# Optimization experiments

Measured on AMD Instinct MI355X. Metric: run time of the kernel, lower is better.

The kernel has to match this reference:

```python
import jax, jax.numpy as jnp
import numpy as np

DECAY = 0.99
EPS = 1e-5
BETA = 0.25

def _l2norm(v, axis=-1):
    # F.normalize: x / max(||x||, 1e-12)
    n = jnp.sqrt(jnp.sum(v * v, axis=axis, keepdims=True))
    return v / jnp.maximum(n, 1e-12)

def setup_inputs() -> dict:
    key = jax.random.key(0)
    k0, k1, k2, k3 = jax.random.split(key, 4)
    B, C, H, W, E, K = 8, 256, 64, 64, 32, 8192
    x = jax.random.normal(k0, (B, C, H, W), jnp.float32)
    Wq = jax.random.normal(k1, (E, C), jnp.float32) * 0.05  # 1x1 conv kernel
    bq = jnp.zeros((E,), jnp.float32)
    emb = jax.random.normal(k2, (K, E), jnp.float32)
    emb = _l2norm(emb, axis=1)  # matches F.normalize init in __init__
    ema_cluster_size = jnp.ones((K,), jnp.float32)
    ema_weight = emb  # consistent post-init EMA state
    return {"x": x, "Wq": Wq, "bq": bq, "embedding": emb,
            "ema_cluster_size": ema_cluster_size, "ema_weight": ema_weight}

def reference(x, Wq, bq, embedding, ema_cluster_size, ema_weight):
    B, C, H, W = x.shape
    E = Wq.shape[0]
    K = embedding.shape[0]
    # quant_conv: 1x1 conv == per-pixel linear
    z = jnp.einsum('bchw,ec->behw', x, Wq) + bq[None, :, None, None]  # [B,E,H,W]
    z_flat = z.transpose(0, 2, 3, 1).reshape(-1, E)  # [N,E]
    # get_idx(use_znorm=True): cosine similarity argmax (== argmin L2 on normalized)
    zn = _l2norm(z_flat, axis=1)
    en = _l2norm(embedding, axis=1)
    indices = jnp.argmax(zn @ en.T, axis=1)  # [N]
    # codebook gather (raw embedding, as in torch)
    z_q = embedding[indices].reshape(B, H, W, E).transpose(0, 3, 1, 2)  # [B,E,H,W]
    # EMA update (training path; scatter == one-hot.T @ z_flat / one-hot.sum)
    counts = jax.ops.segment_sum(jnp.ones((z_flat.shape[0],), z_flat.dtype), indices, num_segments=K)
    dw = jax.ops.segment_sum(z_flat, indices, num_segments=K)  # [K,E]
    new_cs = DECAY * ema_cluster_size + (1.0 - DECAY) * counts
    new_w = DECAY * ema_weight + (1.0 - DECAY) * dw
    n = jnp.sum(new_cs)
    cs_smoothed = (new_cs + EPS) / (n + K * EPS) * n
    new_embedding = new_w / cs_smoothed[:, None]
    # commitment loss + straight-through
    qloss = BETA * jnp.mean((jax.lax.stop_gradient(z_q) - z) ** 2)
    z_q_st = z + jax.lax.stop_gradient(z_q - z)
    return (z_q_st, indices.reshape(B, H, W), qloss, new_embedding, new_cs, new_w)
```

## Files before the change

kernel.cpp:

```cpp
#include <hip/hip_runtime.h>

#define B_ 8
#define C_ 256
#define HW_ 4096
#define E_ 32
#define K_ 8192
#define N_ 32768
#define NCHUNK 4
#define KC_ (K_ / NCHUNK)
#define NSTAGE (KC_ / 128)
#define KSEG 32
#define PIX 128

#define DECAY_ 0.99f
#define OMD_   0.01f
#define EPS_   1e-5f
#define BETA_  0.25f

#define O_ZQ   0
#define O_IDX  1048576
#define O_QL   1081344
#define O_NEMB 1081345
#define O_NCS  1343489
#define O_NW   1351681

#define WS_EH   0u
#define WS_EM   131072u
#define WS_Z    262144u
#define WS_PACK 1310720u
#define WS_PCS  1572864u
#define WS_QP   1572992u

typedef float f32x4 __attribute__((ext_vector_type(4)));
typedef short s16x8 __attribute__((ext_vector_type(8)));
typedef unsigned long long u64;

__device__ __forceinline__ unsigned short f2bf(float f) {
    unsigned u = __float_as_uint(f);
    u = u + 0x7fffu + ((u >> 16) & 1u);
    return (unsigned short)(u >> 16);
}
__device__ __forceinline__ float bf2f(unsigned short h) {
    return __uint_as_float(((unsigned)h) << 16);
}
__device__ __forceinline__ unsigned ford(float f) {
    unsigned u = __float_as_uint(f);
    return (u & 0x80000000u) ? ~u : (u | 0x80000000u);
}
__device__ __forceinline__ int imax(int a, int b) { return a > b ? a : b; }
__device__ __forceinline__ int imin(int a, int b) { return a < b ? a : b; }

__device__ __forceinline__ void gload_lds16(const void* g, void* l) {
    __builtin_amdgcn_global_load_lds(
        (const __attribute__((address_space(1))) unsigned int*)g,
        (__attribute__((address_space(3))) unsigned int*)l, 16, 0, 0);
}

__global__ __launch_bounds__(512) void k_pre(const float* __restrict__ emb,
                                             const float* __restrict__ cs,
                                             uint4* __restrict__ eh16,
                                             uint4* __restrict__ em16,
                                             float* __restrict__ part_cs,
                                             const float* __restrict__ x,
                                             const float* __restrict__ Wq,
                                             const float* __restrict__ bq,
                                             float* __restrict__ zout) {
    __shared__ float wqt[C_ * E_];
    __shared__ float red8[8];
    int tid = threadIdx.x;

    if (blockIdx.x < 16) {
        int k = blockIdx.x * 512 + tid;
        const float4* r = (const float4*)(emb + (size_t)k * E_);
        float v[E_];
        float ss = 0.f;
#pragma unroll
        for (int i = 0; i < 8; i++) {
            float4 t = r[i];
            v[i*4+0] = t.x; v[i*4+1] = t.y; v[i*4+2] = t.z; v[i*4+3] = t.w;
            ss += t.x*t.x + t.y*t.y + t.z*t.z + t.w*t.w;
        }
        float inv = 1.0f / fmaxf(sqrtf(ss), 1e-12f);
        unsigned short h1a[E_], h2a[E_];
#pragma unroll
        for (int e = 0; e < E_; e++) {
            float en = v[e] * inv;
            unsigned short h1 = f2bf(en);
            float r1 = en - bf2f(h1);
            h1a[e] = h1; h2a[e] = f2bf(r1);
        }
        int t = k >> 4, c15 = k & 15;
#pragma unroll
        for (int i = 0; i < 4; i++) {
            eh16[t * 64 + i * 16 + c15] = ((uint4*)h1a)[i];
            em16[t * 64 + i * 16 + c15] = ((uint4*)h2a)[i];
        }

        float cv = cs[blockIdx.x * 512 + tid];
#pragma unroll
        for (int off = 32; off > 0; off >>= 1) cv += __shfl_down(cv, off);
        int lane = tid & 63, wid = tid >> 6;
        if (lane == 0) red8[wid] = cv;
        __syncthreads();
        if (tid == 0) {
            float s = 0.f;
#pragma unroll
            for (int i = 0; i < 8; i++) s += red8[i];
            part_cs[blockIdx.x] = s;
        }
        return;
    }

    int zb = blockIdx.x - 16;
#pragma unroll
    for (int i = 0; i < 16; i++) {
        int g = i * 512 + tid;
        int e = g >> 8;
        int c = g & 255;
        wqt[c * E_ + e] = Wq[g];
    }
    __syncthreads();
    int lp = tid & 63, eg = tid >> 6;
    int n0 = zb * 128 + lp;
    int b  = n0 >> 12, hw = n0 & (HW_ - 1);
    const float* xp = x + (size_t)b * C_ * HW_ + hw;
    float a[8];
#pragma unroll
    for (int j = 0; j < 8; j++) a[j] = 0.f;
#pragma unroll 4
    for (int c = 0; c < C_; c++) {
        float xa = xp[(size_t)c * HW_];
        float xb = xp[(size_t)c * HW_ + 64];
        float4 wv = *(const float4*)(wqt + c * E_ + eg * 4);
        a[0] += xa * wv.x; a[1] += xa * wv.y; a[2] += xa * wv.z; a[3] += xa * wv.w;
        a[4] += xb * wv.x; a[5] += xb * wv.y; a[6] += xb * wv.z; a[7] += xb * wv.w;
    }
    float bq0 = bq[eg*4+0], bq1v = bq[eg*4+1], bq2v = bq[eg*4+2], bq3 = bq[eg*4+3];
    *(float4*)(zout + (size_t)n0 * E_ + eg * 4) =
        make_float4(a[0]+bq0, a[1]+bq1v, a[2]+bq2v, a[3]+bq3);
    *(float4*)(zout + (size_t)(n0 + 64) * E_ + eg * 4) =
        make_float4(a[4]+bq0, a[5]+bq1v, a[6]+bq2v, a[7]+bq3);
}

__global__ __launch_bounds__(512) void k_score_mfma(const float* __restrict__ zws,
                                                    const char* __restrict__ ehb,
                                                    const char* __restrict__ emb_b,
                                                    int2* __restrict__ pk2) {
    __shared__ __align__(16) char smem[32768];

    int tid  = threadIdx.x;
    int lane = tid & 63;
    int w    = tid >> 6;
    int chunk = blockIdx.y;

    s16x8 a1, a2;
    {
        int ploc = w * 16 + (lane & 15);
        int n0   = blockIdx.x * PIX + ploc;
        int e0   = (lane >> 4) * 8;
        const float4* zp = (const float4*)(zws + (size_t)n0 * E_ + e0);
        float4 z0 = zp[0], z1 = zp[1];
        float zz[8] = {z0.x, z0.y, z0.z, z0.w, z1.x, z1.y, z1.z, z1.w};
#pragma unroll
        for (int j = 0; j < 8; j++) {
            float zv = zz[j] * 134217728.0f;
            unsigned short h1 = f2bf(zv);
            float r1 = zv - bf2f(h1);
            a1[j] = (short)h1; a2[j] = (short)f2bf(r1);
        }
    }

    const char* srcp[2];
#pragma unroll
    for (int i = 0; i < 2; i++) {
        int d = i * 512 + tid;
        int pl = d >> 9, dd = d & 511;
        srcp[i] = (pl ? emb_b : ehb) + (size_t)chunk * (KC_ * 64) + dd * 16;
    }

#pragma unroll
    for (int i = 0; i < 2; i++)
        gload_lds16(srcp[i], smem + (i * 512 + tid) * 16);
    __syncthreads();

    int rbase = 8191 - chunk * KC_ - (lane & 15);
    int bq1[4], bq2[4];
#pragma unroll
    for (int j = 0; j < 4; j++) { bq1[j] = (int)0x80000000; bq2[j] = (int)0x80000000; }
    f32x4 zero4 = {0.f, 0.f, 0.f, 0.f};

    for (int st = 0; st < NSTAGE; st++) {
        if (st + 1 < NSTAGE) {
            char* dst = smem + ((st + 1) & 1) * 16384;
#pragma unroll
            for (int i = 0; i < 2; i++)
                gload_lds16(srcp[i] + (size_t)(st + 1) * 8192, dst + (i * 512 + tid) * 16);
        }
        const char* cur = smem + (st & 1) * 16384;
        int rst = rbase - st * 128;

#pragma unroll
        for (int g = 0; g < 2; g++) {
            int ct = g * 4;
            s16x8 b1[4], b2[4];
#pragma unroll
            for (int q = 0; q < 4; q++) {
                b1[q] = ((const s16x8*)(cur +        (ct + q) * 1024))[lane];
                b2[q] = ((const s16x8*)(cur + 8192 + (ct + q) * 1024))[lane];
            }
            f32x4 acc[4];
#pragma unroll
            for (int q = 0; q < 4; q++)
                acc[q] = __builtin_amdgcn_mfma_f32_16x16x32_bf16(a1, b1[q], zero4, 0, 0, 0);
#pragma unroll
            for (int q = 0; q < 4; q++)
                acc[q] = __builtin_amdgcn_mfma_f32_16x16x32_bf16(a1, b2[q], acc[q], 0, 0, 0);
#pragma unroll
            for (int q = 0; q < 4; q++)
                acc[q] = __builtin_amdgcn_mfma_f32_16x16x32_bf16(a2, b1[q], acc[q], 0, 0, 0);
            int r0 = rst - ct * 16;
#pragma unroll
            for (int j = 0; j < 4; j++) {
                int v0 = ((int)acc[0][j] & (int)0xFFFFE000) | r0;
                int v1 = ((int)acc[1][j] & (int)0xFFFFE000) | (r0 - 16);
                int v2 = ((int)acc[2][j] & (int)0xFFFFE000) | (r0 - 32);
                int v3 = ((int)acc[3][j] & (int)0xFFFFE000) | (r0 - 48);
                int hi = imax(imax(v0, v1), imax(v2, v3));
                int m  = imin(bq1[j], hi);
                bq1[j] = imax(bq1[j], hi);
                bq2[j] = imax(bq2[j], m);
            }
        }
        __syncthreads();
    }

#pragma unroll
    for (int off = 1; off < 16; off <<= 1) {
#pragma unroll
        for (int j = 0; j < 4; j++) {
            int o1 = __shfl_xor(bq1[j], off, 64);
            int o2 = __shfl_xor(bq2[j], off, 64);
            int m  = imin(bq1[j], o1);
            bq1[j] = imax(bq1[j], o1);
            bq2[j] = imax(imax(bq2[j], o2), m);
        }
    }
    if ((lane & 15) == 0) {
        int rowbase = blockIdx.x * PIX + w * 16 + (lane >> 4) * 4;
#pragma unroll
        for (int j = 0; j < 4; j++)
            pk2[(size_t)chunk * N_ + rowbase + j] = make_int2(bq1[j], bq2[j]);
    }
}

__device__ __forceinline__ float rescore(const float* __restrict__ emb, int k,
                                         const float* zrow) {
    const float4* r = (const float4*)(emb + (size_t)k * E_);
    float4 v[8];
    float ss = 0.f;
#pragma unroll
    for (int i = 0; i < 8; i++) {
        v[i] = r[i];
        ss += v[i].x * v[i].x + v[i].y * v[i].y + v[i].z * v[i].z + v[i].w * v[i].w;
    }
    float inv = 1.0f / fmaxf(sqrtf(ss), 1e-12f);
    const float4* zp = (const float4*)zrow;
    float sx = 0.f, sy = 0.f, sz = 0.f, sw = 0.f;
#pragma unroll
    for (int i = 0; i < 8; i++) {
        float4 e4 = make_float4(v[i].x * inv, v[i].y * inv, v[i].z * inv, v[i].w * inv);
        float4 zr = zp[i];
        sx += zr.x * e4.x; sy += zr.y * e4.y;
        sz += zr.z * e4.z; sw += zr.w * e4.w;
    }
    return (sx + sy) + (sz + sw);
}

__global__ __launch_bounds__(256) void k_scatter(const float* __restrict__ zws,
                                                 const int2* __restrict__ pk2,
                                                 const float* __restrict__ emb,
                                                 float* __restrict__ out_zq,
                                                 float* __restrict__ out_idx,
                                                 float* __restrict__ qpart) {
    __shared__ float zbuf[32 * E_];
    __shared__ int   idxs_s[32];
    __shared__ float red[4];
    int tid = threadIdx.x;

    const float4* zsrc = (const float4*)(zws + (size_t)blockIdx.x * 32 * E_);
    ((float4*)zbuf)[tid] = zsrc[tid];
    __syncthreads();

    {
        int p = tid >> 3, c8 = tid & 7;
        int chunk = c8 >> 1, top = c8 & 1;
        int nn = blockIdx.x * 32 + p;
        int2 c2 = pk2[(size_t)chunk * N_ + nn];
        int raw = top ? c2.y : c2.x;
        int k = 8191 - (raw & 0x1fff);
        k = k < 0 ? 0 : (k > K_ - 1 ? K_ - 1 : k);
        float s = rescore(emb, k, zbuf + p * E_);
        u64 pkd = ((u64)ford(s) << 32) | (unsigned)(K_ - 1 - k);
        u64 o = __shfl_xor(pkd, 1, 64); pkd = pkd > o ? pkd : o;
        o = __shfl_xor(pkd, 2, 64);     pkd = pkd > o ? pkd : o;
        o = __shfl_xor(pkd, 4, 64);     pkd = pkd > o ? pkd : o;
        if (c8 == 0) {
            int bi = K_ - 1 - (int)(unsigned)(pkd & 0xffffffffu);
            idxs_s[p] = bi;
            out_idx[nn] = (float)bi;
        }
    }
    __syncthreads();

    int lp = tid & 31, eg = tid >> 5;
    int n  = blockIdx.x * 32 + lp;
    int b  = n >> 12, hw = n & (HW_ - 1);
    int idx = idxs_s[lp];
    float4 e4 = *(const float4*)(emb + (size_t)idx * E_ + eg * 4);
    float* o = out_zq + (size_t)b * E_ * HW_ + (size_t)(eg * 4) * HW_ + hw;

    float z0 = zbuf[lp * E_ + eg * 4 + 0];
    float z1 = zbuf[lp * E_ + eg * 4 + 1];
    float z2 = zbuf[lp * E_ + eg * 4 + 2];
    float z3 = zbuf[lp * E_ + eg * 4 + 3];
    o[0]                 = e4.x;
    o[(size_t)1 * HW_]   = e4.y;
    o[(size_t)2 * HW_]   = e4.z;
    o[(size_t)3 * HW_]   = e4.w;
    float d0 = e4.x - z0, d1 = e4.y - z1, d2 = e4.z - z2, d3 = e4.w - z3;
    float sq = d0*d0 + d1*d1 + d2*d2 + d3*d3;

#pragma unroll
    for (int off = 32; off > 0; off >>= 1) sq += __shfl_down(sq, off);
    int lane = tid & 63, wid = tid >> 6;
    if (lane == 0) red[wid] = sq;
    __syncthreads();
    if (tid == 0) qpart[blockIdx.x] = red[0] + red[1] + red[2] + red[3];
}

__global__ __launch_bounds__(256) void k_dwfinal(const float* __restrict__ zws,
                                                 const float* __restrict__ idxf,
                                                 const float* __restrict__ cs,
                                                 const float* __restrict__ ew,
                                                 const float* __restrict__ part_cs,
                                                 const float* __restrict__ qpart,
                                                 float* __restrict__ out_nw,
                                                 float* __restrict__ out_nemb,
                                                 float* __restrict__ out_ncs,
                                                 float* __restrict__ out_ql) {
    __shared__ float acc[KSEG * E_];
    __shared__ int   cnt_s[KSEG];
    __shared__ int   plist[2048];
    __shared__ int   lcnt;
    __shared__ float nsum_s;
    int tid = threadIdx.x;
    int kbase = blockIdx.x * KSEG;

#pragma unroll
    for (int i = 0; i < KSEG * E_ / 256; i++) acc[tid + i * 256] = 0.f;
    if (tid < KSEG) cnt_s[tid] = 0;
    if (tid == 0) lcnt = 0;
    __syncthreads();

    const float4* idx4 = (const float4*)idxf;
    for (int tile = 0; tile < N_ / 2048; ++tile) {
        int pbase = tile * 2048 + tid * 8;
        float4 f0 = idx4[tile * 512 + tid * 2];
        float4 f1 = idx4[tile * 512 + tid * 2 + 1];
        float fs[8] = {f0.x, f0.y, f0.z, f0.w, f1.x, f1.y, f1.z, f1.w};
#pragma unroll
        for (int s = 0; s < 8; s++) {
            unsigned d = (unsigned)((int)fs[s] - kbase);
            if (d < (unsigned)KSEG) {
                int pos = atomicAdd(&lcnt, 1);
                plist[pos] = ((pbase + s) << 5) | (int)d;
                atomicAdd(cnt_s + (int)d, 1);
            }
        }
        __syncthreads();
        int cnt = lcnt;
        int e = tid & 31;
        for (int m = tid >> 5; m < cnt; m += 8) {
            int pk = plist[m];
            int nn = pk >> 5;
            float zv = zws[(size_t)nn * E_ + e];
            atomicAdd(acc + (pk & 31) * E_ + e, zv);
        }
        __syncthreads();
        if (tid == 0) lcnt = 0;
        __syncthreads();
    }

    if (tid < 64) {
        float s = (tid < 16) ? part_cs[tid] : 0.f;
        s += __shfl_down(s, 8);
        s += __shfl_down(s, 4);
        s += __shfl_down(s, 2);
        s += __shfl_down(s, 1);
        if (tid == 0) nsum_s = DECAY_ * s + OMD_ * (float)N_;
    }
    __syncthreads();
    float nsum = nsum_s;

#pragma unroll
    for (int i = 0; i < 4; i++) {
        int local = tid + i * 256;
        int kl = local >> 5, c = local & 31;
        int k = kbase + kl;
        float v = DECAY_ * ew[(size_t)k * E_ + c] + OMD_ * acc[local];
        out_nw[(size_t)k * E_ + c] = v;
        float csk = DECAY_ * cs[k] + OMD_ * (float)cnt_s[kl];
        float denom = (csk + EPS_) / (nsum + (float)K_ * EPS_) * nsum;
        out_nemb[(size_t)k * E_ + c] = v / denom;
        if (c == 0) out_ncs[k] = csk;
    }

    if (blockIdx.x == 0 && tid < 64) {
        float s = 0.f;
#pragma unroll
        for (int i = 0; i < 16; i++) s += qpart[tid + i * 64];
#pragma unroll
        for (int off = 32; off > 0; off >>= 1) s += __shfl_down(s, off);
        if (tid == 0) out_ql[0] = BETA_ * s / (float)(B_ * E_ * HW_);
    }
}

extern "C" void kernel_launch(void* const* d_in, const int* in_sizes, int n_in,
                              void* d_out, int out_size, void* d_ws, size_t ws_size,
                              hipStream_t stream) {
    const float* x   = (const float*)d_in[0];
    const float* Wq  = (const float*)d_in[1];
    const float* bq  = (const float*)d_in[2];
    const float* emb = (const float*)d_in[3];
    const float* cs  = (const float*)d_in[4];
    const float* ew  = (const float*)d_in[5];
    float* out = (float*)d_out;
    float* ws  = (float*)d_ws;

    k_pre<<<16 + N_ / 128, 512, 0, stream>>>(emb, cs,
        (uint4*)(ws + WS_EH), (uint4*)(ws + WS_EM), ws + WS_PCS,
        x, Wq, bq, ws + WS_Z);
    k_score_mfma<<<dim3(N_ / PIX, NCHUNK), 512, 0, stream>>>(ws + WS_Z,
        (const char*)(ws + WS_EH), (const char*)(ws + WS_EM),
        (int2*)(ws + WS_PACK));
    k_scatter<<<N_ / 32, 256, 0, stream>>>(ws + WS_Z,
        (const int2*)(ws + WS_PACK), emb,
        out + O_ZQ, out + O_IDX, ws + WS_QP);
    k_dwfinal<<<K_ / KSEG, 256, 0, stream>>>(ws + WS_Z, out + O_IDX, cs, ew,
                                             ws + WS_PCS, ws + WS_QP,
                                             out + O_NW, out + O_NEMB,
                                             out + O_NCS, out + O_QL);
}
```

Before: 198.0 us.

## Fuse codebook scoring with rescoring and scatter, drop codebook chunk split

Removes the 4-way split of the codebook across grid.y so each block scans all 8192 codes. The fp32 rescore, index write, z_q scatter and loss partial then run in the same kernel from shared memory, which removes the packed-candidate workspace round trip and one launch. The cost is a grid four times smaller (256 blocks) with four times longer serial stage loops, which may leave the GPU underoccupied. The 1x1 conv loop unroll also goes from 4 to 8.

Result: slower. 209.7 us (+5.9%).

```diff
diff --git a/kernel.cpp b/kernel.cpp
--- a/kernel.cpp
+++ b/kernel.cpp
@@ -6,9 +6,7 @@
 #define E_ 32
 #define K_ 8192
 #define N_ 32768
-#define NCHUNK 4
-#define KC_ (K_ / NCHUNK)
-#define NSTAGE (KC_ / 128)
+#define NSTAGE (K_ / 128)
 #define KSEG 32
 #define PIX 128
 
@@ -27,9 +25,8 @@
 #define WS_EH   0u
 #define WS_EM   131072u
 #define WS_Z    262144u
-#define WS_PACK 1310720u
-#define WS_PCS  1572864u
-#define WS_QP   1572992u
+#define WS_PCS  1310720u
+#define WS_QP   1310736u
 
 typedef float f32x4 __attribute__((ext_vector_type(4)));
 typedef short s16x8 __attribute__((ext_vector_type(8)));
@@ -127,7 +124,7 @@
     float a[8];
 #pragma unroll
     for (int j = 0; j < 8; j++) a[j] = 0.f;
-#pragma unroll 4
+#pragma unroll 8
     for (int c = 0; c < C_; c++) {
         float xa = xp[(size_t)c * HW_];
         float xb = xp[(size_t)c * HW_ + 64];
@@ -142,16 +139,44 @@
         make_float4(a[4]+bq0, a[5]+bq1v, a[6]+bq2v, a[7]+bq3);
 }
 
-__global__ __launch_bounds__(512) void k_score_mfma(const float* __restrict__ zws,
-                                                    const char* __restrict__ ehb,
-                                                    const char* __restrict__ emb_b,
-                                                    int2* __restrict__ pk2) {
+__device__ __forceinline__ float rescore(const float* __restrict__ emb, int k,
+                                         const float* zrow) {
+    const float4* r = (const float4*)(emb + (size_t)k * E_);
+    float4 v[8];
+    float ss = 0.f;
+#pragma unroll
+    for (int i = 0; i < 8; i++) {
+        v[i] = r[i];
+        ss += v[i].x * v[i].x + v[i].y * v[i].y + v[i].z * v[i].z + v[i].w * v[i].w;
+    }
+    float inv = 1.0f / fmaxf(sqrtf(ss), 1e-12f);
+    const float4* zp = (const float4*)zrow;
+    float sx = 0.f, sy = 0.f, sz = 0.f, sw = 0.f;
+#pragma unroll
+    for (int i = 0; i < 8; i++) {
+        float4 e4 = make_float4(v[i].x * inv, v[i].y * inv, v[i].z * inv, v[i].w * inv);
+        float4 zr = zp[i];
+        sx += zr.x * e4.x; sy += zr.y * e4.y;
+        sz += zr.z * e4.z; sw += zr.w * e4.w;
+    }
+    return (sx + sy) + (sz + sw);
+}
+
+__global__ __launch_bounds__(512) void k_score_fused(const float* __restrict__ zws,
+                                                     const char* __restrict__ ehb,
+                                                     const char* __restrict__ emb_b,
+                                                     const float* __restrict__ emb,
+                                                     float* __restrict__ out_zq,
+                                                     float* __restrict__ out_idx,
+                                                     float* __restrict__ qpart) {
     __shared__ __align__(16) char smem[32768];
+    __shared__ float zbuf[PIX * E_];
+    __shared__ int2  t2[PIX];
+    __shared__ float red8[8];
 
     int tid  = threadIdx.x;
     int lane = tid & 63;
     int w    = tid >> 6;
-    int chunk = blockIdx.y;
 
     s16x8 a1, a2;
     {
@@ -160,6 +185,8 @@
         int e0   = (lane >> 4) * 8;
         const float4* zp = (const float4*)(zws + (size_t)n0 * E_ + e0);
         float4 z0 = zp[0], z1 = zp[1];
+        *(float4*)(zbuf + ploc * E_ + e0)     = z0;
+        *(float4*)(zbuf + ploc * E_ + e0 + 4) = z1;
         float zz[8] = {z0.x, z0.y, z0.z, z0.w, z1.x, z1.y, z1.z, z1.w};
 #pragma unroll
         for (int j = 0; j < 8; j++) {
@@ -175,7 +202,7 @@
     for (int i = 0; i < 2; i++) {
         int d = i * 512 + tid;
         int pl = d >> 9, dd = d & 511;
-        srcp[i] = (pl ? emb_b : ehb) + (size_t)chunk * (KC_ * 64) + dd * 16;
+        srcp[i] = (pl ? emb_b : ehb) + dd * 16;
     }
 
 #pragma unroll
@@ -183,7 +210,7 @@
         gload_lds16(srcp[i], smem + (i * 512 + tid) * 16);
     __syncthreads();
 
-    int rbase = 8191 - chunk * KC_ - (lane & 15);
+    int rbase = 8191 - (lane & 15);
     int bq1[4], bq2[4];
 #pragma unroll
     for (int j = 0; j < 4; j++) { bq1[j] = (int)0x80000000; bq2[j] = (int)0x80000000; }
@@ -246,96 +273,59 @@
         }
     }
     if ((lane & 15) == 0) {
-        int rowbase = blockIdx.x * PIX + w * 16 + (lane >> 4) * 4;
+        int rowb = w * 16 + (lane >> 4) * 4;
 #pragma unroll
         for (int j = 0; j < 4; j++)
-            pk2[(size_t)chunk * N_ + rowbase + j] = make_int2(bq1[j], bq2[j]);
-    }
-}
-
-__device__ __forceinline__ float rescore(const float* __restrict__ emb, int k,
-                                         const float* zrow) {
-    const float4* r = (const float4*)(emb + (size_t)k * E_);
-    float4 v[8];
-    float ss = 0.f;
-#pragma unroll
-    for (int i = 0; i < 8; i++) {
-        v[i] = r[i];
-        ss += v[i].x * v[i].x + v[i].y * v[i].y + v[i].z * v[i].z + v[i].w * v[i].w;
-    }
-    float inv = 1.0f / fmaxf(sqrtf(ss), 1e-12f);
-    const float4* zp = (const float4*)zrow;
-    float sx = 0.f, sy = 0.f, sz = 0.f, sw = 0.f;
-#pragma unroll
-    for (int i = 0; i < 8; i++) {
-        float4 e4 = make_float4(v[i].x * inv, v[i].y * inv, v[i].z * inv, v[i].w * inv);
-        float4 zr = zp[i];
-        sx += zr.x * e4.x; sy += zr.y * e4.y;
-        sz += zr.z * e4.z; sw += zr.w * e4.w;
-    }
-    return (sx + sy) + (sz + sw);
-}
-
-__global__ __launch_bounds__(256) void k_scatter(const float* __restrict__ zws,
-                                                 const int2* __restrict__ pk2,
-                                                 const float* __restrict__ emb,
-                                                 float* __restrict__ out_zq,
-                                                 float* __restrict__ out_idx,
-                                                 float* __restrict__ qpart) {
-    __shared__ float zbuf[32 * E_];
-    __shared__ int   idxs_s[32];
-    __shared__ float red[4];
-    int tid = threadIdx.x;
-
-    const float4* zsrc = (const float4*)(zws + (size_t)blockIdx.x * 32 * E_);
-    ((float4*)zbuf)[tid] = zsrc[tid];
+            t2[rowb + j] = make_int2(bq1[j], bq2[j]);
+    }
     __syncthreads();
 
     {
-        int p = tid >> 3, c8 = tid & 7;
-        int chunk = c8 >> 1, top = c8 & 1;
-        int nn = blockIdx.x * 32 + p;
-        int2 c2 = pk2[(size_t)chunk * N_ + nn];
-        int raw = top ? c2.y : c2.x;
+        int p = tid >> 2, c4 = tid & 3;
+        int2 c2 = t2[p];
+        int raw = (c4 & 1) ? c2.y : c2.x;
         int k = 8191 - (raw & 0x1fff);
         k = k < 0 ? 0 : (k > K_ - 1 ? K_ - 1 : k);
         float s = rescore(emb, k, zbuf + p * E_);
         u64 pkd = ((u64)ford(s) << 32) | (unsigned)(K_ - 1 - k);
         u64 o = __shfl_xor(pkd, 1, 64); pkd = pkd > o ? pkd : o;
         o = __shfl_xor(pkd, 2, 64);     pkd = pkd > o ? pkd : o;
-        o = __shfl_xor(pkd, 4, 64);     pkd = pkd > o ? pkd : o;
-        if (c8 == 0) {
+        if (c4 == 0) {
             int bi = K_ - 1 - (int)(unsigned)(pkd & 0xffffffffu);
-            idxs_s[p] = bi;
-            out_idx[nn] = (float)bi;
-        }
-    }
-    __syncthreads();
-
-    int lp = tid & 31, eg = tid >> 5;
-    int n  = blockIdx.x * 32 + lp;
-    int b  = n >> 12, hw = n & (HW_ - 1);
-    int idx = idxs_s[lp];
-    float4 e4 = *(const float4*)(emb + (size_t)idx * E_ + eg * 4);
-    float* o = out_zq + (size_t)b * E_ * HW_ + (size_t)(eg * 4) * HW_ + hw;
-
-    float z0 = zbuf[lp * E_ + eg * 4 + 0];
-    float z1 = zbuf[lp * E_ + eg * 4 + 1];
-    float z2 = zbuf[lp * E_ + eg * 4 + 2];
-    float z3 = zbuf[lp * E_ + eg * 4 + 3];
-    o[0]                 = e4.x;
-    o[(size_t)1 * HW_]   = e4.y;
-    o[(size_t)2 * HW_]   = e4.z;
-    o[(size_t)3 * HW_]   = e4.w;
-    float d0 = e4.x - z0, d1 = e4.y - z1, d2 = e4.z - z2, d3 = e4.w - z3;
-    float sq = d0*d0 + d1*d1 + d2*d2 + d3*d3;
-
-#pragma unroll
-    for (int off = 32; off > 0; off >>= 1) sq += __shfl_down(sq, off);
-    int lane = tid & 63, wid = tid >> 6;
-    if (lane == 0) red[wid] = sq;
-    __syncthreads();
-    if (tid == 0) qpart[blockIdx.x] = red[0] + red[1] + red[2] + red[3];
+            ((int*)t2)[p * 2] = bi;
+            out_idx[blockIdx.x * PIX + p] = (float)bi;
+        }
+    }
+    __syncthreads();
+
+    {
+        int px = tid & 127, eg = tid >> 7;
+        int n  = blockIdx.x * PIX + px;
+        int b  = n >> 12, hw = n & (HW_ - 1);
+        int idx = ((int*)t2)[px * 2];
+        const float* er = emb + (size_t)idx * E_ + eg * 8;
+        float* o = out_zq + (size_t)b * E_ * HW_ + (size_t)(eg * 8) * HW_ + hw;
+
+        float sq = 0.f;
+#pragma unroll
+        for (int j = 0; j < 8; j++) {
+            float zv = zbuf[px * E_ + eg * 8 + j];
+            float qf = er[j];
+            float d = qf - zv;
+            sq += d * d;
+            o[(size_t)j * HW_] = qf;
+        }
+#pragma unroll
+        for (int off = 32; off > 0; off >>= 1) sq += __shfl_down(sq, off);
+        if (lane == 0) red8[w] = sq;
+        __syncthreads();
+        if (tid == 0) {
+            float s = 0.f;
+#pragma unroll
+            for (int i = 0; i < 8; i++) s += red8[i];
+            qpart[blockIdx.x] = s;
+        }
+    }
 }
 
 __global__ __launch_bounds__(256) void k_dwfinal(const float* __restrict__ zws,
@@ -418,7 +408,7 @@
     if (blockIdx.x == 0 && tid < 64) {
         float s = 0.f;
 #pragma unroll
-        for (int i = 0; i < 16; i++) s += qpart[tid + i * 64];
+        for (int i = 0; i < 4; i++) s += qpart[tid + i * 64];
 #pragma unroll
         for (int off = 32; off > 0; off >>= 1) s += __shfl_down(s, off);
         if (tid == 0) out_ql[0] = BETA_ * s / (float)(B_ * E_ * HW_);
@@ -440,11 +430,8 @@
     k_pre<<<16 + N_ / 128, 512, 0, stream>>>(emb, cs,
         (uint4*)(ws + WS_EH), (uint4*)(ws + WS_EM), ws + WS_PCS,
         x, Wq, bq, ws + WS_Z);
-    k_score_mfma<<<dim3(N_ / PIX, NCHUNK), 512, 0, stream>>>(ws + WS_Z,
-        (const char*)(ws + WS_EH), (const char*)(ws + WS_EM),
-        (int2*)(ws + WS_PACK));
-    k_scatter<<<N_ / 32, 256, 0, stream>>>(ws + WS_Z,
-        (const int2*)(ws + WS_PACK), emb,
+    k_score_fused<<<N_ / PIX, 512, 0, stream>>>(ws + WS_Z,
+        (const char*)(ws + WS_EH), (const char*)(ws + WS_EM), emb,
         out + O_ZQ, out + O_IDX, ws + WS_QP);
     k_dwfinal<<<K_ / KSEG, 256, 0, stream>>>(ws + WS_Z, out + O_IDX, cs, ew,
                                              ws + WS_PCS, ws + WS_QP,
```
